# Optimization experiments

Measured on AMD Instinct MI355X. Metric: run time of the kernel, lower is better.

## Reference

```python
import jax, jax.numpy as jnp
import numpy as np

N_QUBITS = 7
N_LAYERS = 4
DIM = 2 ** N_QUBITS  # 128
# PennyLane StronglyEntanglingLayers default ranges: (l % (n_wires-1)) + 1
RANGES = [(l % (N_QUBITS - 1)) + 1 for l in range(N_LAYERS)]  # [1,2,3,4]
BATCH = 262144


def rot_matrix(phi, theta, omega):
    """PennyLane Rot(phi, theta, omega) = RZ(omega) RY(theta) RZ(phi)."""
    c = jnp.cos(theta / 2)
    s = jnp.sin(theta / 2)
    a = jnp.exp(-0.5j * (phi + omega)) * c
    b = -jnp.exp(0.5j * (phi - omega)) * s
    cc = jnp.exp(-0.5j * (phi - omega)) * s
    d = jnp.exp(0.5j * (phi + omega)) * c
    return jnp.stack([jnp.stack([a, b]), jnp.stack([cc, d])])  # (2,2) complex64


def apply_1q(psi, U, wire):
    # psi: (batch, 2,2,2,2,2,2,2); apply 2x2 U on qubit axis 1+wire
    psi = jnp.moveaxis(psi, 1 + wire, -1)
    psi = psi @ U.T
    return jnp.moveaxis(psi, -1, 1 + wire)


def apply_cnot(psi, ctrl, tgt):
    psi = jnp.moveaxis(psi, (1 + ctrl, 1 + tgt), (-2, -1))
    # flip target amplitude pair where control == 1
    psi = jnp.concatenate([psi[..., 0:1, :], psi[..., 1:2, ::-1]], axis=-2)
    return jnp.moveaxis(psi, (-2, -1), (1 + ctrl, 1 + tgt))


def setup_inputs() -> dict:
    key = jax.random.key(0)
    k1, k2 = jax.random.split(key)
    x = jax.random.normal(k1, (BATCH, DIM), dtype=jnp.float32)
    weights = jax.random.normal(k2, (N_LAYERS, N_QUBITS, 3), dtype=jnp.float32)
    return {"x": x, "weights": weights}


def reference(x, weights):
    # AmplitudeEmbedding with normalize=True
    norm = jnp.linalg.norm(x, axis=-1, keepdims=True)
    psi = (x / norm).astype(jnp.complex64)
    psi = psi.reshape((-1,) + (2,) * N_QUBITS)

    # StronglyEntanglingLayers
    for l in range(N_LAYERS):
        for w in range(N_QUBITS):
            U = rot_matrix(weights[l, w, 0], weights[l, w, 1], weights[l, w, 2])
            psi = apply_1q(psi, U, w)
        r = RANGES[l]
        for w in range(N_QUBITS):
            psi = apply_cnot(psi, w, (w + r) % N_QUBITS)

    # expval(Z0 @ Z6): sign = (-1)^(b0 + b6)
    probs = (jnp.abs(psi) ** 2).reshape(-1, 2, DIM // 4, 2)  # (batch, q0, mid, q6)
    z = jnp.array([1.0, -1.0], dtype=jnp.float32)
    return jnp.einsum('a,namb,b->n', z, probs, z)
```

## Files before the change

kernel.cpp:

```cpp
#include <hip/hip_runtime.h>


#define N_QUBITS 7
#define DIM 128
#define N_LAYERS 4
#define BATCH 262144
#define NT (BATCH / 64)

typedef short short8 __attribute__((ext_vector_type(8)));
typedef float f32x4 __attribute__((ext_vector_type(4)));

__device__ __forceinline__ unsigned short f2bf(float f) {
  unsigned u = __builtin_bit_cast(unsigned, f);
  u += 0x7fffu + ((u >> 16) & 1u);
  return (unsigned short)(u >> 16);
}

__device__ __forceinline__ short8 pack_bf16(float4 a, float4 b) {
  short8 r;
  r[0] = (short)f2bf(a.x); r[1] = (short)f2bf(a.y);
  r[2] = (short)f2bf(a.z); r[3] = (short)f2bf(a.w);
  r[4] = (short)f2bf(b.x); r[5] = (short)f2bf(b.y);
  r[6] = (short)f2bf(b.z); r[7] = (short)f2bf(b.w);
  return r;
}

__global__ void sim_columns(const float* __restrict__ W,
                            float* __restrict__ Ur, float* __restrict__ Ui) {
  __shared__ float sr[DIM], si[DIM];
  const int c = blockIdx.x;
  const int t = threadIdx.x;

  sr[t] = (t == c) ? 1.f : 0.f;        si[t] = 0.f;
  sr[t + 64] = (t + 64 == c) ? 1.f : 0.f;  si[t + 64] = 0.f;
  __syncthreads();

  for (int l = 0; l < N_LAYERS; ++l) {
    for (int w = 0; w < N_QUBITS; ++w) {
      const float phi = W[(l * 7 + w) * 3 + 0];
      const float th  = W[(l * 7 + w) * 3 + 1];
      const float om  = W[(l * 7 + w) * 3 + 2];
      const float ch = __cosf(0.5f * th), sh = __sinf(0.5f * th);
      const float ap = 0.5f * (phi + om), am = 0.5f * (phi - om);
      const float cap = __cosf(ap), sap = __sinf(ap);
      const float cam = __cosf(am), sam = __sinf(am);
      const float ar =  cap * ch, ai = -sap * ch;
      const float br = -cam * sh, bi = -sam * sh;
      const float cr =  cam * sh, ci = -sam * sh;
      const float dr =  cap * ch, di =  sap * ch;

      const int m = 1 << (6 - w);
      const int i0 = ((t & ~(m - 1)) << 1) | (t & (m - 1));
      const int i1 = i0 | m;
      const float x0r = sr[i0], x0i = si[i0];
      const float x1r = sr[i1], x1i = si[i1];
      __syncthreads();
      sr[i0] = ar * x0r - ai * x0i + br * x1r - bi * x1i;
      si[i0] = ar * x0i + ai * x0r + br * x1i + bi * x1r;
      sr[i1] = cr * x0r - ci * x0i + dr * x1r - di * x1i;
      si[i1] = cr * x0i + ci * x0r + dr * x1i + di * x1r;
      __syncthreads();
    }
    const int r = (l % (N_QUBITS - 1)) + 1;
    for (int w = 0; w < N_QUBITS; ++w) {
      const int ctrl = w, tgt = (w + r) % N_QUBITS;
      const int cmask = 1 << (6 - ctrl), tmask = 1 << (6 - tgt);
      const int i0 = ((t & ~(tmask - 1)) << 1) | (t & (tmask - 1));
      const int i1 = i0 | tmask;
      const float a0r = sr[i0], a0i = si[i0];
      const float a1r = sr[i1], a1i = si[i1];
      __syncthreads();
      if (i0 & cmask) {
        sr[i0] = a1r; si[i0] = a1i;
        sr[i1] = a0r; si[i1] = a0i;
      }
      __syncthreads();
    }
  }
  Ur[(size_t)t * DIM + c]        = sr[t];
  Ui[(size_t)t * DIM + c]        = si[t];
  Ur[(size_t)(t + 64) * DIM + c] = sr[t + 64];
  Ui[(size_t)(t + 64) * DIM + c] = si[t + 64];
}

__global__ void build_A(const float* __restrict__ Ur, const float* __restrict__ Ui,
                        unsigned short* __restrict__ Ab) {
  const int idx = blockIdx.x * blockDim.x + threadIdx.x;
  const int i = idx >> 7, j = idx & 127;
  float s = 0.f;
#pragma unroll 4
  for (int k = 0; k < DIM; ++k) {
    const float zk = (((k >> 6) ^ k) & 1) ? -1.f : 1.f;
    s += zk * (Ur[k * DIM + i] * Ur[k * DIM + j] + Ui[k * DIM + i] * Ui[k * DIM + j]);
  }
  Ab[idx] = f2bf(s);
}

__global__ __launch_bounds__(256, 2) void vqa_main(const float* __restrict__ X,
                                                   const unsigned short* __restrict__ Ab,
                                                   float* __restrict__ out) {
  const int lane = threadIdx.x & 63;
  const int wave = threadIdx.x >> 6;
  const int n16 = lane & 15;
  const int g = lane >> 4;

  short8 afrag[8][4];
#pragma unroll
  for (int t = 0; t < 8; ++t)
#pragma unroll
    for (int kt = 0; kt < 4; ++kt)
      afrag[t][kt] =
          *reinterpret_cast<const short8*>(Ab + (t * 16 + n16) * DIM + kt * 32 + g * 8);

  int tile = blockIdx.x;
  if (tile >= NT) return;

  float4 xb[8];
  {
    const float* xp = X + (size_t)(tile * 64 + wave * 16 + n16) * DIM + g * 8;
#pragma unroll
    for (int kt = 0; kt < 4; ++kt) {
      xb[2 * kt]     = *reinterpret_cast<const float4*>(xp + kt * 32);
      xb[2 * kt + 1] = *reinterpret_cast<const float4*>(xp + kt * 32 + 4);
    }
  }

  while (true) {
    const int n = tile * 64 + wave * 16 + n16;

    short8 bfrag[4];
#pragma unroll
    for (int kt = 0; kt < 4; ++kt) bfrag[kt] = pack_bf16(xb[2 * kt], xb[2 * kt + 1]);

    const int next = tile + gridDim.x;
    if (next < NT) {
      const float* xq = X + (size_t)(next * 64 + wave * 16 + n16) * DIM + g * 8;
#pragma unroll
      for (int kt = 0; kt < 4; ++kt) {
        xb[2 * kt]     = *reinterpret_cast<const float4*>(xq + kt * 32);
        xb[2 * kt + 1] = *reinterpret_cast<const float4*>(xq + kt * 32 + 4);
      }
    }

    f32x4 acc[8];
#pragma unroll
    for (int t = 0; t < 8; ++t) acc[t] = (f32x4){0.f, 0.f, 0.f, 0.f};
#pragma unroll
    for (int kt = 0; kt < 4; ++kt)
#pragma unroll
      for (int t = 0; t < 8; ++t)
        acc[t] = __builtin_amdgcn_mfma_f32_16x16x32_bf16(afrag[t][kt], bfrag[kt],
                                                         acc[t], 0, 0, 0);

    const float* xe = X + (size_t)n * DIM + g * 4;
    float dot = 0.f, nrm = 0.f;
#pragma unroll
    for (int t = 0; t < 8; ++t) {
      const float4 xr = *reinterpret_cast<const float4*>(xe + t * 16);
      dot += xr.x * acc[t][0] + xr.y * acc[t][1] + xr.z * acc[t][2] + xr.w * acc[t][3];
      nrm += xr.x * xr.x + xr.y * xr.y + xr.z * xr.z + xr.w * xr.w;
    }
    dot += __shfl_xor(dot, 16, 64);
    dot += __shfl_xor(dot, 32, 64);
    nrm += __shfl_xor(nrm, 16, 64);
    nrm += __shfl_xor(nrm, 32, 64);
    if (lane < 16) out[n] = dot / nrm;

    if (next >= NT) break;
    tile = next;
  }
}

extern "C" void kernel_launch(void* const* d_in, const int* in_sizes, int n_in,
                              void* d_out, int out_size, void* d_ws, size_t ws_size,
                              hipStream_t stream) {
  const float* X = (const float*)d_in[0];
  const float* W = (const float*)d_in[1];
  float* out = (float*)d_out;

  float* Ur = (float*)d_ws;
  float* Ui = Ur + DIM * DIM;
  unsigned short* Ab = (unsigned short*)(Ui + DIM * DIM);

  sim_columns<<<DIM, 64, 0, stream>>>(W, Ur, Ui);
  build_A<<<64, 256, 0, stream>>>(Ur, Ui, Ab);
  vqa_main<<<512, 256, 0, stream>>>(X, Ab, out);
}
```

Before: 217.8 us.

## Stage A matrix in swizzled LDS instead of registers, raise occupancy

```diff
diff --git a/kernel.cpp b/kernel.cpp
--- a/kernel.cpp
+++ b/kernel.cpp
@@ -96,61 +96,55 @@
   Ab[idx] = f2bf(s);
 }
 
-__global__ __launch_bounds__(256, 2) void vqa_main(const float* __restrict__ X,
+__global__ __launch_bounds__(256, 4) void vqa_main(const float* __restrict__ X,
                                                    const unsigned short* __restrict__ Ab,
                                                    float* __restrict__ out) {
-  const int lane = threadIdx.x & 63;
-  const int wave = threadIdx.x >> 6;
+  __shared__ unsigned short As[DIM * DIM];
+
+  const int tid = threadIdx.x;
+  const int lane = tid & 63;
+  const int wave = tid >> 6;
   const int n16 = lane & 15;
   const int g = lane >> 4;
 
-  short8 afrag[8][4];
 #pragma unroll
-  for (int t = 0; t < 8; ++t)
+  for (int i = 0; i < 8; ++i) {
+    const int q = tid + 256 * i;
+    const int m = q >> 4, c = q & 15;
+    const short8 v = *reinterpret_cast<const short8*>(Ab + q * 8);
+    *reinterpret_cast<short8*>(As + m * DIM + ((c ^ (m & 15)) << 3)) = v;
+  }
+  __syncthreads();
+
+  const unsigned short* abase[4];
 #pragma unroll
-    for (int kt = 0; kt < 4; ++kt)
-      afrag[t][kt] =
-          *reinterpret_cast<const short8*>(Ab + (t * 16 + n16) * DIM + kt * 32 + g * 8);
+  for (int kt = 0; kt < 4; ++kt)
+    abase[kt] = As + n16 * DIM + ((((4 * kt + g) ^ n16)) << 3);
 
-  int tile = blockIdx.x;
-  if (tile >= NT) return;
+  for (int tile = blockIdx.x; tile < NT; tile += gridDim.x) {
+    const int n = tile * 64 + wave * 16 + n16;
 
-  float4 xb[8];
-  {
-    const float* xp = X + (size_t)(tile * 64 + wave * 16 + n16) * DIM + g * 8;
+    const float* xp = X + (size_t)n * DIM + g * 8;
+    short8 bfrag[4];
 #pragma unroll
     for (int kt = 0; kt < 4; ++kt) {
-      xb[2 * kt]     = *reinterpret_cast<const float4*>(xp + kt * 32);
-      xb[2 * kt + 1] = *reinterpret_cast<const float4*>(xp + kt * 32 + 4);
-    }
-  }
-
-  while (true) {
-    const int n = tile * 64 + wave * 16 + n16;
-
-    short8 bfrag[4];
-#pragma unroll
-    for (int kt = 0; kt < 4; ++kt) bfrag[kt] = pack_bf16(xb[2 * kt], xb[2 * kt + 1]);
-
-    const int next = tile + gridDim.x;
-    if (next < NT) {
-      const float* xq = X + (size_t)(next * 64 + wave * 16 + n16) * DIM + g * 8;
-#pragma unroll
-      for (int kt = 0; kt < 4; ++kt) {
-        xb[2 * kt]     = *reinterpret_cast<const float4*>(xq + kt * 32);
-        xb[2 * kt + 1] = *reinterpret_cast<const float4*>(xq + kt * 32 + 4);
-      }
+      const float4 lo = *reinterpret_cast<const float4*>(xp + kt * 32);
+      const float4 hi = *reinterpret_cast<const float4*>(xp + kt * 32 + 4);
+      bfrag[kt] = pack_bf16(lo, hi);
     }
 
     f32x4 acc[8];
 #pragma unroll
     for (int t = 0; t < 8; ++t) acc[t] = (f32x4){0.f, 0.f, 0.f, 0.f};
+
 #pragma unroll
-    for (int kt = 0; kt < 4; ++kt)
+    for (int kt = 0; kt < 4; ++kt) {
 #pragma unroll
-      for (int t = 0; t < 8; ++t)
-        acc[t] = __builtin_amdgcn_mfma_f32_16x16x32_bf16(afrag[t][kt], bfrag[kt],
-                                                         acc[t], 0, 0, 0);
+      for (int t = 0; t < 8; ++t) {
+        const short8 af = *reinterpret_cast<const short8*>(abase[kt] + t * 16 * DIM);
+        acc[t] = __builtin_amdgcn_mfma_f32_16x16x32_bf16(af, bfrag[kt], acc[t], 0, 0, 0);
+      }
+    }
 
     const float* xe = X + (size_t)n * DIM + g * 4;
     float dot = 0.f, nrm = 0.f;
@@ -165,9 +159,6 @@
     nrm += __shfl_xor(nrm, 16, 64);
     nrm += __shfl_xor(nrm, 32, 64);
     if (lane < 16) out[n] = dot / nrm;
-
-    if (next >= NT) break;
-    tile = next;
   }
 }
 
@@ -184,5 +175,5 @@
 
   sim_columns<<<DIM, 64, 0, stream>>>(W, Ur, Ui);
   build_A<<<64, 256, 0, stream>>>(Ur, Ui, Ab);
-  vqa_main<<<512, 256, 0, stream>>>(X, Ab, out);
+  vqa_main<<<1024, 256, 0, stream>>>(X, Ab, out);
 }
```

Measured after the change: 262.3 us. +20.4%, slower.
